# Kernel tuning notes

Measured on AMD Instinct MI355X. Metric: run time of the kernel, lower is better.

Reference implementation:

```python
import jax, jax.numpy as jnp
import numpy as np

N_NODES = 10000
AVG_DEG = 16
N_EDGES = N_NODES * AVG_DEG
NODE_DIM, EDGE_DIM, LIN_DIM, HID, OUT, LAYERS = 9, 3, 32, 300, 2, 5


def _init(key, shape, fan_in):
    return jax.random.normal(key, shape, jnp.float32) * (1.0 / np.sqrt(fan_in))


def setup_inputs() -> dict:
    key = jax.random.key(0)
    ks = jax.random.split(key, 18)
    inp = {
        "x": jax.random.normal(ks[0], (N_NODES, NODE_DIM), jnp.float32),
        "edge_index": jax.random.randint(ks[1], (2, N_EDGES), 0, N_NODES, jnp.int32),
        "edge_attr": jax.random.normal(ks[2], (N_EDGES, EDGE_DIM), jnp.float32),
        "batch": jnp.zeros((N_NODES,), jnp.int32),
        # nn.Linear params (stored as [in, out] so fwd is x @ W + b)
        "node_w": _init(ks[3], (NODE_DIM, LIN_DIM), NODE_DIM),
        "node_b": jnp.zeros((LIN_DIM,), jnp.float32),
        "edge_w": _init(ks[4], (EDGE_DIM, LIN_DIM), EDGE_DIM),
        "edge_b": jnp.zeros((LIN_DIM,), jnp.float32),
        # GCNConv: lin (no bias) + separate additive bias (PyG convention)
        "gcn0_w": _init(ks[5], (LIN_DIM, HID), LIN_DIM),
        "gcn0_b": jnp.zeros((HID,), jnp.float32),
        "gcn_w": _init(ks[6], (LAYERS - 1, HID, HID), HID),
        "gcn_b": jnp.zeros((LAYERS - 1, HID), jnp.float32),
        "lin1_w": _init(ks[7], (HID, LIN_DIM), HID),
        "lin1_b": jnp.zeros((LIN_DIM,), jnp.float32),
        "lin2_w": _init(ks[8], (LIN_DIM, OUT), LIN_DIM),
        "lin2_b": jnp.zeros((OUT,), jnp.float32),
    }
    return inp


def reference(x, edge_index, edge_attr, batch,
              node_w, node_b, edge_w, edge_b,
              gcn0_w, gcn0_b, gcn_w, gcn_b,
              lin1_w, lin1_b, lin2_w, lin2_b):
    row, col = edge_index[0], edge_index[1]

    e = edge_attr @ edge_w + edge_b  # [E, LIN_DIM] edge embeddings

    # Faithful to the original bug: node embeddings get edge attrs scatter-added,
    # then the result is discarded by `attr = edge_attr`. Kept for fidelity (dead).
    node_h = x @ node_w + node_b
    node_h = node_h.at[row].add(e)  # unused downstream

    # GCN stack runs over the E-row edge-embedding matrix -> effective node count = E
    h = e
    n = h.shape[0]  # == N_EDGES

    # symmetric gcn_norm with self-loops (edge_weight = 1), computed once
    deg = jax.ops.segment_sum(jnp.ones((edge_index.shape[1],), h.dtype), col,
                              num_segments=n) + 1.0
    dinv = jax.lax.rsqrt(deg)
    norm = dinv[row] * dinv[col]  # per-edge normalization
    self_norm = (dinv * dinv)[:, None]  # self-loop term

    def gcn(h, w, b):
        hw = h @ w  # dense transform
        agg = jax.ops.segment_sum(hw[row] * norm[:, None], col, num_segments=n)
        return agg + self_norm * hw + b

    h = jax.nn.relu(gcn(h, gcn0_w, gcn0_b))

    def step(h, wb):
        w, b = wb
        return jax.nn.relu(gcn(h, w, b)), None

    h, _ = jax.lax.scan(step, h, (gcn_w, gcn_b))

    g = jnp.mean(h, axis=0, keepdims=True)  # [1, HID] graph readout
    g = jax.nn.relu(g @ lin1_w + lin1_b)
    pred = g @ lin2_w + lin2_b  # [1, OUT]; forward returns pre-softmax logits
    return pred
```

## Files before the change

kernel.cpp:

```cpp
#include <hip/hip_runtime.h>
#include <hip/hip_bf16.h>

#define N_NODES 10000
#define N_EDGES 160000
#define HID 300
#define HIDP 304
#define NPARTB (N_EDGES - N_NODES)
#define KS 328
#define RBM 80
#define RBF 16
#define PARTB_BLOCKS 1875
#define GEMMA_BLOCKS 125
#define FILL_BLOCKS 313
#define MEGA_BLOCKS (PARTB_BLOCKS + GEMMA_BLOCKS + FILL_BLOCKS)
#define FUSE_BLOCKS 625

typedef __attribute__((ext_vector_type(8))) short short8;
typedef __attribute__((ext_vector_type(4))) short s16x4;
typedef __attribute__((ext_vector_type(4))) float f32x4;

#define MFMA_B16(a, b, c) __builtin_amdgcn_mfma_f32_16x16x32_bf16(a, b, c, 0, 0, 0)

__device__ __forceinline__ short bf16r(float x) {
    unsigned u = __float_as_uint(x);
    return (short)((u + 0x7fffu + ((u >> 16) & 1u)) >> 16);
}
__device__ __forceinline__ float b2f(unsigned short u) {
    return __uint_as_float(((unsigned)u) << 16);
}
__device__ __forceinline__ void split1(float x, short& hi, short& lo) {
    short h = bf16r(x);
    float hf = __uint_as_float(((unsigned)(unsigned short)h) << 16);
    hi = h;
    lo = bf16r(x - hf);
}

__global__ void k_prep(const float* __restrict__ g0w, const float* __restrict__ gw,
                       short* __restrict__ wt0, short* __restrict__ wtl,
                       const int* __restrict__ col, int* __restrict__ cnt) {
    int idx = blockIdx.x * 256 + threadIdx.x;
    if (idx < N_EDGES) atomicAdd(&cnt[col[idx]], 1);
    if (idx < 1216) {
        int n16 = idx & 15, q = (idx >> 4) & 3, nt = idx >> 6;
        int n = nt * 16 + n16;
        short* hd = wt0 + (size_t)(nt * 8 + q) * 128 + n16 * 8;
        short* ld = wt0 + (size_t)(nt * 8 + 4 + q) * 128 + n16 * 8;
#pragma unroll
        for (int j = 0; j < 8; ++j) {
            int k = q * 8 + j;
            float f = (n < HID) ? g0w[k * HID + n] : 0.0f;
            short hi, lo;
            split1(f, hi, lo);
            hd[j] = hi;
            ld[j] = lo;
        }
    } else if (idx < 1216 + 48640) {
        int i = idx - 1216;
        int n16 = i & 15; i >>= 4;
        int q = i & 3; i >>= 2;
        int nt = i % 19; i /= 19;
        int chunk = i % 10;
        int l = i / 10;
        int n = nt * 16 + n16;
        int cnt_idx = chunk * 19 + nt;
        short* base = wtl + (size_t)l * 194560;
        short* hd = base + (size_t)(cnt_idx * 8 + q) * 128 + n16 * 8;
        short* ld = base + (size_t)(cnt_idx * 8 + 4 + q) * 128 + n16 * 8;
#pragma unroll
        for (int j = 0; j < 8; ++j) {
            int k = chunk * 32 + q * 8 + j;
            float f = (k < HID && n < HID) ? gw[((size_t)l * HID + k) * HID + n] : 0.0f;
            short hi, lo;
            split1(f, hi, lo);
            hd[j] = hi;
            ld[j] = lo;
        }
    }
}

__global__ __launch_bounds__(1024) void k_scan(
    const int* __restrict__ cnt, int* __restrict__ col_start,
    int* __restrict__ cursor, float* __restrict__ dinv,
    float* __restrict__ selfnorm) {
    __shared__ int wsum[16];
    int t = threadIdx.x;
    int lane = t & 63, w = t >> 6;
    int carry = 0;
    for (int base = 0; base < N_NODES; base += 1024) {
        int i = base + t;
        int v = (i < N_NODES) ? cnt[i] : 0;
        int s = v;
#pragma unroll
        for (int d = 1; d < 64; d <<= 1) {
            int n = __shfl_up(s, d, 64);
            if (lane >= d) s += n;
        }
        if (lane == 63) wsum[w] = s;
        __syncthreads();
        int woff = 0, total = 0;
#pragma unroll
        for (int k = 0; k < 16; ++k) {
            if (k < w) woff += wsum[k];
            total += wsum[k];
        }
        if (i < N_NODES) {
            int excl = carry + woff + s - v;
            col_start[i] = excl;
            cursor[i] = excl;
            float dd = (float)v + 1.0f;
            dinv[i] = rsqrtf(dd);
            selfnorm[i] = 1.0f / dd;
        }
        carry += total;
        __syncthreads();
    }
    if (t == 0) col_start[N_NODES] = carry;
}

template <int MT, int NTC>
__device__ __forceinline__ void kloop(const short* __restrict__ wp, int nch,
                                      const short* Hh, int nt0, int quad, int l16,
                                      f32x4 (&acc)[MT][NTC]) {
#pragma unroll
    for (int mt = 0; mt < MT; ++mt)
#pragma unroll
        for (int i = 0; i < NTC; ++i)
#pragma unroll
            for (int r = 0; r < 4; ++r) acc[mt][i][r] = 0.0f;
#pragma unroll 1
    for (int c = 0; c < nch; ++c) {
        const short* cb = wp + (size_t)(c * 19 + nt0) * 1024 + quad * 128 + l16 * 8;
        short8 ah[MT];
#pragma unroll
        for (int mt = 0; mt < MT; ++mt)
            ah[mt] = *(const short8*)&Hh[(mt * 16 + l16) * KS + c * 32 + quad * 8];
        short8 bb[NTC];
#pragma unroll
        for (int i = 0; i < NTC; ++i) bb[i] = *(const short8*)(cb + (size_t)i * 1024);
#pragma unroll
        for (int mt = 0; mt < MT; ++mt)
#pragma unroll
            for (int i = 0; i < NTC; ++i)
                acc[mt][i] = MFMA_B16(ah[mt], bb[i], acc[mt][i]);
#pragma unroll
        for (int i = 0; i < NTC; ++i) bb[i] = *(const short8*)(cb + (size_t)i * 1024 + 512);
#pragma unroll
        for (int mt = 0; mt < MT; ++mt)
#pragma unroll
            for (int i = 0; i < NTC; ++i)
                acc[mt][i] = MFMA_B16(ah[mt], bb[i], acc[mt][i]);
    }
}

template <int MT, int NTC>
__device__ __forceinline__ void kloop_p(const short* __restrict__ wp, int nch,
                                        const short* Hh, int nt0, int quad, int l16,
                                        f32x4 (&acc)[MT][NTC]) {
#pragma unroll
    for (int mt = 0; mt < MT; ++mt)
#pragma unroll
        for (int i = 0; i < NTC; ++i)
#pragma unroll
            for (int r = 0; r < 4; ++r) acc[mt][i][r] = 0.0f;

    const short* a0 = Hh + l16 * KS + quad * 8;
    const short* w0 = wp + (size_t)nt0 * 1024 + (size_t)(quad * 128 + l16 * 8);

    short8 ah[MT], an[MT], b1[NTC], b1n[NTC], b2[NTC];
#pragma unroll
    for (int mt = 0; mt < MT; ++mt) ah[mt] = *(const short8*)(a0 + mt * 16 * KS);
#pragma unroll
    for (int i = 0; i < NTC; ++i) b1[i] = *(const short8*)(w0 + (size_t)i * 1024);

#pragma unroll 1
    for (int c = 0; c < nch - 1; ++c) {
        const short* wc = w0 + (size_t)c * 19456;
        const short* wn = wc + 19456;
        const short* apn = a0 + (c + 1) * 32;
#pragma unroll
        for (int i = 0; i < NTC; ++i) b2[i] = *(const short8*)(wc + (size_t)i * 1024 + 512);
#pragma unroll
        for (int mt = 0; mt < MT; ++mt) an[mt] = *(const short8*)(apn + mt * 16 * KS);
#pragma unroll
        for (int i = 0; i < NTC; ++i) b1n[i] = *(const short8*)(wn + (size_t)i * 1024);
#pragma unroll
        for (int mt = 0; mt < MT; ++mt)
#pragma unroll
            for (int i = 0; i < NTC; ++i) acc[mt][i] = MFMA_B16(ah[mt], b1[i], acc[mt][i]);
#pragma unroll
        for (int mt = 0; mt < MT; ++mt)
#pragma unroll
            for (int i = 0; i < NTC; ++i) acc[mt][i] = MFMA_B16(ah[mt], b2[i], acc[mt][i]);
#pragma unroll
        for (int mt = 0; mt < MT; ++mt) ah[mt] = an[mt];
#pragma unroll
        for (int i = 0; i < NTC; ++i) b1[i] = b1n[i];
    }
    {
        const short* wc = w0 + (size_t)(nch - 1) * 19456;
#pragma unroll
        for (int i = 0; i < NTC; ++i) b2[i] = *(const short8*)(wc + (size_t)i * 1024 + 512);
#pragma unroll
        for (int mt = 0; mt < MT; ++mt)
#pragma unroll
            for (int i = 0; i < NTC; ++i) acc[mt][i] = MFMA_B16(ah[mt], b1[i], acc[mt][i]);
#pragma unroll
        for (int mt = 0; mt < MT; ++mt)
#pragma unroll
            for (int i = 0; i < NTC; ++i) acc[mt][i] = MFMA_B16(ah[mt], b2[i], acc[mt][i]);
    }
}

template <int MT, int NTC>
__device__ __forceinline__ void gcn_epilogue(const float* __restrict__ bias,
                                             int nt0, int quad, int l16,
                                             f32x4 (&acc)[MT][NTC], short* Hh) {
#pragma unroll
    for (int i = 0; i < NTC; ++i) {
        int c = (nt0 + i) * 16 + l16;
        float b = (c < HID) ? bias[c] : 0.0f;
#pragma unroll
        for (int mt = 0; mt < MT; ++mt)
#pragma unroll
            for (int r = 0; r < 4; ++r) {
                float v = fmaxf(acc[mt][i][r] + b, 0.0f);
                Hh[(mt * 16 + quad * 4 + r) * KS + c] = bf16r(v);
            }
    }
}

template <int MT, int NTC>
__device__ __forceinline__ void gcn_final(const float* __restrict__ bias,
                                          int nt0, int quad, int l16,
                                          f32x4 (&acc)[MT][NTC],
                                          float* __restrict__ gout) {
#pragma unroll
    for (int i = 0; i < NTC; ++i) {
        int c = (nt0 + i) * 16 + l16;
        float b = (c < HID) ? bias[c] : 0.0f;
        float s = 0.0f;
#pragma unroll
        for (int mt = 0; mt < MT; ++mt)
#pragma unroll
            for (int r = 0; r < 4; ++r) s += fmaxf(acc[mt][i][r] + b, 0.0f);
        s += __shfl_xor(s, 16, 64);
        s += __shfl_xor(s, 32, 64);
        if (quad == 0) gout[c] = (c < HID) ? s : 0.0f;
    }
}

template <int MT, int NTC>
__device__ __forceinline__ void gemm_out(int base, int nt0, int quad, int l16,
                                         f32x4 (&acc)[MT][NTC],
                                         unsigned short* __restrict__ HW) {
#pragma unroll
    for (int i = 0; i < NTC; ++i) {
        int c = (nt0 + i) * 16 + l16;
#pragma unroll
        for (int mt = 0; mt < MT; ++mt)
#pragma unroll
            for (int r = 0; r < 4; ++r) {
                int gm = base + mt * 16 + quad * 4 + r;
                if (gm < N_NODES)
                    HW[(size_t)gm * HIDP + c] = (unsigned short)bf16r(acc[mt][i][r]);
            }
    }
}

__global__ __launch_bounds__(512, 4) void k_mega(
    const float* __restrict__ edge_attr,
    const float* __restrict__ edge_w,
    const float* __restrict__ edge_b,
    const short* __restrict__ wt0,
    const short* __restrict__ wtl,
    const float* __restrict__ gcn0_b,
    const float* __restrict__ gcn_b,
    float* __restrict__ gpartB,
    unsigned short* __restrict__ hw0,
    const int* __restrict__ row,
    const int* __restrict__ col,
    int* __restrict__ cursor,
    const float* __restrict__ dinv,
    int2* __restrict__ edge_pack) {
    __shared__ short Hh[RBM * KS];
    int bid = blockIdx.x, t = threadIdx.x;
    int lane = t & 63, w = t >> 6;
    int l16 = lane & 15, quad = lane >> 4;
    int nt0 = (w < 3) ? w * 3 : 9 + (w - 3) * 2;

    if (bid < PARTB_BLOCKS) {
        int base = N_NODES + bid * RBM;
        for (int i = t; i < RBM * 8; i += 512) {
            int r = i >> 3, c4 = (i & 7) * 4;
            const float* ar = edge_attr + (size_t)(base + r) * 3;
            float a0 = ar[0], a1 = ar[1], a2 = ar[2];
#pragma unroll
            for (int j = 0; j < 4; ++j) {
                int cc = c4 + j;
                float v = edge_b[cc];
                v = fmaf(a0, edge_w[cc], v);
                v = fmaf(a1, edge_w[32 + cc], v);
                v = fmaf(a2, edge_w[64 + cc], v);
                Hh[r * KS + cc] = bf16r(v);
            }
        }
        for (int i = t; i < RBM * 24; i += 512) {
            int r = i / 24, k = 304 + i % 24;
            Hh[r * KS + k] = 0;
        }
        __syncthreads();

        float* gout = gpartB + (size_t)bid * HIDP;
        if (w < 3) {
            f32x4 acc[5][3];
            kloop<5, 3>(wt0, 1, Hh, nt0, quad, l16, acc);
            __syncthreads();
            gcn_epilogue<5, 3>(gcn0_b, nt0, quad, l16, acc, Hh);
            __syncthreads();
            for (int l = 0; l < 4; ++l) {
                kloop<5, 3>(wtl + (size_t)l * 194560, 10, Hh, nt0, quad, l16, acc);
                __syncthreads();
                if (l < 3) {
                    gcn_epilogue<5, 3>(gcn_b + l * HID, nt0, quad, l16, acc, Hh);
                    __syncthreads();
                } else {
                    gcn_final<5, 3>(gcn_b + l * HID, nt0, quad, l16, acc, gout);
                }
            }
        } else {
            f32x4 acc[5][2];
            kloop<5, 2>(wt0, 1, Hh, nt0, quad, l16, acc);
            __syncthreads();
            gcn_epilogue<5, 2>(gcn0_b, nt0, quad, l16, acc, Hh);
            __syncthreads();
            for (int l = 0; l < 4; ++l) {
                kloop<5, 2>(wtl + (size_t)l * 194560, 10, Hh, nt0, quad, l16, acc);
                __syncthreads();
                if (l < 3) {
                    gcn_epilogue<5, 2>(gcn_b + l * HID, nt0, quad, l16, acc, Hh);
                    __syncthreads();
                } else {
                    gcn_final<5, 2>(gcn_b + l * HID, nt0, quad, l16, acc, gout);
                }
            }
        }
    } else if (bid < PARTB_BLOCKS + GEMMA_BLOCKS) {
        int base = (bid - PARTB_BLOCKS) * RBM;
        for (int i = t; i < RBM * 8; i += 512) {
            int r = i >> 3, c4 = (i & 7) * 4;
            const float* ar = edge_attr + (size_t)(base + r) * 3;
            float a0 = ar[0], a1 = ar[1], a2 = ar[2];
#pragma unroll
            for (int j = 0; j < 4; ++j) {
                int cc = c4 + j;
                float v = edge_b[cc];
                v = fmaf(a0, edge_w[cc], v);
                v = fmaf(a1, edge_w[32 + cc], v);
                v = fmaf(a2, edge_w[64 + cc], v);
                Hh[r * KS + cc] = bf16r(v);
            }
        }
        for (int i = t; i < RBM * 24; i += 512) {
            int r = i / 24, k = 304 + i % 24;
            Hh[r * KS + k] = 0;
        }
        __syncthreads();
        if (w < 3) {
            f32x4 acc[5][3];
            kloop<5, 3>(wt0, 1, Hh, nt0, quad, l16, acc);
            gemm_out<5, 3>(base, nt0, quad, l16, acc, hw0);
        } else {
            f32x4 acc[5][2];
            kloop<5, 2>(wt0, 1, Hh, nt0, quad, l16, acc);
            gemm_out<5, 2>(base, nt0, quad, l16, acc, hw0);
        }
    } else {
        int e = (bid - PARTB_BLOCKS - GEMMA_BLOCKS) * 512 + t;
        if (e < N_EDGES) {
            int c = col[e], r = row[e];
            int p = atomicAdd(&cursor[c], 1);
            edge_pack[p] = make_int2(r, __float_as_int(dinv[r] * dinv[c]));
        }
    }
}

__device__ __forceinline__ void agg_edge4(int i, int lane, int cap,
                                          const unsigned short* __restrict__ hw_in,
                                          const int2* __restrict__ ep,
                                          float (&v)[5]) {
    int2 e0 = ep[i], e1 = ep[i + 1], e2 = ep[i + 2], e3 = ep[i + 3];
    const unsigned short* h0 = hw_in + (size_t)e0.x * HIDP;
    const unsigned short* h1 = hw_in + (size_t)e1.x * HIDP;
    const unsigned short* h2 = hw_in + (size_t)e2.x * HIDP;
    const unsigned short* h3 = hw_in + (size_t)e3.x * HIDP;
    float n0 = __int_as_float(e0.y), n1 = __int_as_float(e1.y);
    float n2 = __int_as_float(e2.y), n3 = __int_as_float(e3.y);
#pragma unroll
    for (int jj = 0; jj < 5; ++jj) {
        int cc = lane + 64 * jj;
        if (cc < cap) {
            float s = v[jj];
            s = fmaf(n0, b2f(h0[cc]), s);
            s = fmaf(n1, b2f(h1[cc]), s);
            s = fmaf(n2, b2f(h2[cc]), s);
            s = fmaf(n3, b2f(h3[cc]), s);
            v[jj] = s;
        }
    }
}

__device__ __forceinline__ void agg_pair(int c0, int c1, int lane,
                                         const unsigned short* __restrict__ hw_in,
                                         const int* __restrict__ col_start,
                                         const int2* __restrict__ ep,
                                         float (&v0)[5], float (&v1)[5]) {
#pragma unroll
    for (int jj = 0; jj < 5; ++jj) { v0[jj] = 0.0f; v1[jj] = 0.0f; }
    int i0 = col_start[c0], e0 = col_start[c0 + 1];
    int i1 = col_start[c1], e1 = col_start[c1 + 1];
#pragma unroll 1
    while (i0 + 4 <= e0 && i1 + 4 <= e1) {
        int2 a0 = ep[i0], a1 = ep[i0 + 1], a2 = ep[i0 + 2], a3 = ep[i0 + 3];
        int2 b0 = ep[i1], b1 = ep[i1 + 1], b2 = ep[i1 + 2], b3 = ep[i1 + 3];
        const unsigned short* pa0 = hw_in + (size_t)a0.x * HIDP;
        const unsigned short* pa1 = hw_in + (size_t)a1.x * HIDP;
        const unsigned short* pa2 = hw_in + (size_t)a2.x * HIDP;
        const unsigned short* pa3 = hw_in + (size_t)a3.x * HIDP;
        const unsigned short* pb0 = hw_in + (size_t)b0.x * HIDP;
        const unsigned short* pb1 = hw_in + (size_t)b1.x * HIDP;
        const unsigned short* pb2 = hw_in + (size_t)b2.x * HIDP;
        const unsigned short* pb3 = hw_in + (size_t)b3.x * HIDP;
        float na0 = __int_as_float(a0.y), na1 = __int_as_float(a1.y);
        float na2 = __int_as_float(a2.y), na3 = __int_as_float(a3.y);
        float nb0 = __int_as_float(b0.y), nb1 = __int_as_float(b1.y);
        float nb2 = __int_as_float(b2.y), nb3 = __int_as_float(b3.y);
#pragma unroll
        for (int jj = 0; jj < 5; ++jj) {
            int cc = lane + 64 * jj;
            if (cc < HIDP) {
                float s = v0[jj];
                s = fmaf(na0, b2f(pa0[cc]), s);
                s = fmaf(na1, b2f(pa1[cc]), s);
                s = fmaf(na2, b2f(pa2[cc]), s);
                s = fmaf(na3, b2f(pa3[cc]), s);
                v0[jj] = s;
                float u = v1[jj];
                u = fmaf(nb0, b2f(pb0[cc]), u);
                u = fmaf(nb1, b2f(pb1[cc]), u);
                u = fmaf(nb2, b2f(pb2[cc]), u);
                u = fmaf(nb3, b2f(pb3[cc]), u);
                v1[jj] = u;
            }
        }
        i0 += 4; i1 += 4;
    }
#pragma unroll 1
    for (; i0 + 4 <= e0; i0 += 4) agg_edge4(i0, lane, HIDP, hw_in, ep, v0);
#pragma unroll 1
    for (; i0 < e0; ++i0) {
        int2 q = ep[i0];
        const unsigned short* h = hw_in + (size_t)q.x * HIDP;
        float n = __int_as_float(q.y);
#pragma unroll
        for (int jj = 0; jj < 5; ++jj) {
            int cc = lane + 64 * jj;
            if (cc < HIDP) v0[jj] = fmaf(n, b2f(h[cc]), v0[jj]);
        }
    }
#pragma unroll 1
    for (; i1 + 4 <= e1; i1 += 4) agg_edge4(i1, lane, HIDP, hw_in, ep, v1);
#pragma unroll 1
    for (; i1 < e1; ++i1) {
        int2 q = ep[i1];
        const unsigned short* h = hw_in + (size_t)q.x * HIDP;
        float n = __int_as_float(q.y);
#pragma unroll
        for (int jj = 0; jj < 5; ++jj) {
            int cc = lane + 64 * jj;
            if (cc < HIDP) v1[jj] = fmaf(n, b2f(h[cc]), v1[jj]);
        }
    }
}

__global__ __launch_bounds__(512, 4) void k_fuse(
    const unsigned short* __restrict__ hw_in,
    const int* __restrict__ col_start,
    const int2* __restrict__ edge_pack,
    const float* __restrict__ selfnorm,
    const float* __restrict__ bias,
    const short* __restrict__ wt,
    unsigned short* __restrict__ hw_out) {
    __shared__ short Hh[RBF * KS];
    int t = threadIdx.x;
    int lane = t & 63, w = t >> 6;
    int l16 = lane & 15, quad = lane >> 4;
    int base = blockIdx.x * RBF;
    int nt0 = (w < 3) ? w * 3 : 9 + (w - 3) * 2;

    {
        int c0 = base + w * 2, c1 = c0 + 1;
        float v0[5], v1[5];
        agg_pair(c0, c1, lane, hw_in, col_start, edge_pack, v0, v1);
        float sn0 = selfnorm[c0], sn1 = selfnorm[c1];
        const unsigned short* sp0 = hw_in + (size_t)c0 * HIDP;
        const unsigned short* sp1 = hw_in + (size_t)c1 * HIDP;
        int r0 = w * 2;
#pragma unroll
        for (int jj = 0; jj < 5; ++jj) {
            int cc = lane + 64 * jj;
            if (cc < HIDP) {
                float b = (cc < HID) ? bias[cc] : 0.0f;
                float h0 = v0[jj] + sn0 * b2f(sp0[cc]) + b;
                float h1 = v1[jj] + sn1 * b2f(sp1[cc]) + b;
                Hh[r0 * KS + cc] = bf16r(fmaxf(h0, 0.0f));
                Hh[(r0 + 1) * KS + cc] = bf16r(fmaxf(h1, 0.0f));
            }
        }
    }
    for (int i = t; i < RBF * 6; i += 512) {
        int r = i / 6, k = 304 + (i % 6) * 4;
        *(s16x4*)&Hh[r * KS + k] = (s16x4)0;
    }
    __syncthreads();

    if (w < 3) {
        f32x4 acc[1][3];
        kloop_p<1, 3>(wt, 10, Hh, nt0, quad, l16, acc);
        gemm_out<1, 3>(base, nt0, quad, l16, acc, hw_out);
    } else {
        f32x4 acc[1][2];
        kloop_p<1, 2>(wt, 10, Hh, nt0, quad, l16, acc);
        gemm_out<1, 2>(base, nt0, quad, l16, acc, hw_out);
    }
}

__global__ __launch_bounds__(512) void k_last(
    const unsigned short* __restrict__ hw_in,
    const int* __restrict__ col_start,
    const int2* __restrict__ edge_pack,
    const float* __restrict__ selfnorm,
    const float* __restrict__ bias,
    const float* __restrict__ gpartB,
    float* __restrict__ g_sum) {
    __shared__ float red[8 * 320];
    int t = threadIdx.x;
    int lane = t & 63, w = t >> 6;
    int base = blockIdx.x * RBF;

    float s[5] = {0.0f, 0.0f, 0.0f, 0.0f, 0.0f};
    {
        int c0 = base + w * 2, c1 = c0 + 1;
        float v0[5], v1[5];
        agg_pair(c0, c1, lane, hw_in, col_start, edge_pack, v0, v1);
        float sn0 = selfnorm[c0], sn1 = selfnorm[c1];
        const unsigned short* sp0 = hw_in + (size_t)c0 * HIDP;
        const unsigned short* sp1 = hw_in + (size_t)c1 * HIDP;
#pragma unroll
        for (int jj = 0; jj < 5; ++jj) {
            int cc = lane + 64 * jj;
            if (cc < HID) {
                float b = bias[cc];
                s[jj] += fmaxf(v0[jj] + sn0 * b2f(sp0[cc]) + b, 0.0f);
                s[jj] += fmaxf(v1[jj] + sn1 * b2f(sp1[cc]) + b, 0.0f);
            }
        }
    }
    if (w < 3) {
        int rr = blockIdx.x * 3 + w;
        if (rr < PARTB_BLOCKS) {
#pragma unroll
            for (int jj = 0; jj < 5; ++jj) {
                int cc = lane + 64 * jj;
                if (cc < HID) s[jj] += gpartB[(size_t)rr * HIDP + cc];
            }
        }
    }
#pragma unroll
    for (int jj = 0; jj < 5; ++jj) red[w * 320 + lane + 64 * jj] = s[jj];
    __syncthreads();
    if (w == 0) {
#pragma unroll
        for (int jj = 0; jj < 5; ++jj) {
            int cc = lane + 64 * jj;
            if (cc < HID) {
                float tot = 0.0f;
#pragma unroll
                for (int g = 0; g < 8; ++g) tot += red[g * 320 + cc];
                atomicAdd(&g_sum[cc], tot);
            }
        }
    }
}

__global__ void k_head(const float* __restrict__ g_sum,
                       const float* __restrict__ lin1_w, const float* __restrict__ lin1_b,
                       const float* __restrict__ lin2_w, const float* __restrict__ lin2_b,
                       float* __restrict__ out) {
    __shared__ float g2[32];
    int t = threadIdx.x;
    const float inv = 1.0f / (float)N_EDGES;
    if (t < 32) {
        float a = lin1_b[t];
        for (int d = 0; d < HID; ++d) a = fmaf(g_sum[d] * inv, lin1_w[d * 32 + t], a);
        g2[t] = fmaxf(a, 0.0f);
    }
    __syncthreads();
    if (t < 2) {
        float p = lin2_b[t];
        for (int j = 0; j < 32; ++j) p = fmaf(g2[j], lin2_w[j * 2 + t], p);
        out[t] = p;
    }
}


extern "C" void kernel_launch(void* const* d_in, const int* in_sizes, int n_in,
                              void* d_out, int out_size, void* d_ws, size_t ws_size,
                              hipStream_t stream) {
    (void)in_sizes; (void)n_in; (void)out_size; (void)ws_size;
    const int* edge_index = (const int*)d_in[1];
    const float* edge_attr = (const float*)d_in[2];
    const float* edge_w = (const float*)d_in[6];
    const float* edge_b = (const float*)d_in[7];
    const float* gcn0_w = (const float*)d_in[8];
    const float* gcn0_b = (const float*)d_in[9];
    const float* gcn_w = (const float*)d_in[10];
    const float* gcn_b = (const float*)d_in[11];
    const float* lin1_w = (const float*)d_in[12];
    const float* lin1_b = (const float*)d_in[13];
    const float* lin2_w = (const float*)d_in[14];
    const float* lin2_b = (const float*)d_in[15];

    char* ws = (char*)d_ws;
    size_t off = 0;
    auto alloc = [&](size_t bytes) {
        void* p = ws + off;
        off = (off + bytes + 255) & ~(size_t)255;
        return p;
    };
    unsigned short* hwA = (unsigned short*)alloc((size_t)N_NODES * HIDP * 2);
    unsigned short* hwB = (unsigned short*)alloc((size_t)N_NODES * HIDP * 2);
    int2* edge_pack = (int2*)alloc((size_t)N_EDGES * 8);
    int* cnt = (int*)alloc((size_t)N_NODES * 4);
    int* col_start = (int*)alloc((size_t)(N_NODES + 1) * 4);
    int* cursor = (int*)alloc((size_t)N_NODES * 4);
    float* dinv = (float*)alloc((size_t)N_NODES * 4);
    float* selfnorm = (float*)alloc((size_t)N_NODES * 4);
    float* g_sum = (float*)alloc((size_t)HIDP * 4);
    short* wt0 = (short*)alloc((size_t)38912);
    short* wtl = (short*)alloc((size_t)4 * 389120);
    float* gpartB = (float*)alloc((size_t)PARTB_BLOCKS * HIDP * 4);

    const int* row = edge_index;
    const int* col = edge_index + N_EDGES;

    hipMemsetAsync(cnt, 0, N_NODES * 4, stream);
    hipMemsetAsync(g_sum, 0, HIDP * 4, stream);

    k_prep<<<(N_EDGES + 255) / 256, 256, 0, stream>>>(gcn0_w, gcn_w, wt0, wtl, col, cnt);
    k_scan<<<1, 1024, 0, stream>>>(cnt, col_start, cursor, dinv, selfnorm);

    k_mega<<<MEGA_BLOCKS, 512, 0, stream>>>(edge_attr, edge_w, edge_b, wt0, wtl,
                                            gcn0_b, gcn_b, gpartB, hwA,
                                            row, col, cursor, dinv, edge_pack);

    k_fuse<<<FUSE_BLOCKS, 512, 0, stream>>>(hwA, col_start, edge_pack, selfnorm,
                                            gcn0_b, wtl + (size_t)0 * 194560, hwB);
    k_fuse<<<FUSE_BLOCKS, 512, 0, stream>>>(hwB, col_start, edge_pack, selfnorm,
                                            gcn_b + 0 * HID, wtl + (size_t)1 * 194560, hwA);
    k_fuse<<<FUSE_BLOCKS, 512, 0, stream>>>(hwA, col_start, edge_pack, selfnorm,
                                            gcn_b + 1 * HID, wtl + (size_t)2 * 194560, hwB);
    k_fuse<<<FUSE_BLOCKS, 512, 0, stream>>>(hwB, col_start, edge_pack, selfnorm,
                                            gcn_b + 2 * HID, wtl + (size_t)3 * 194560, hwA);
    k_last<<<FUSE_BLOCKS, 512, 0, stream>>>(hwA, col_start, edge_pack, selfnorm,
                                            gcn_b + 3 * HID, gpartB, g_sum);
    k_head<<<1, 64, 0, stream>>>(g_sum, lin1_w, lin1_b, lin2_w, lin2_b, (float*)d_out);
}
```

Baseline: 460.1 us.

## Interleave independent partB dense-GCN blocks with the four aggregation layer kernels

```diff
diff --git a/kernel.cpp b/kernel.cpp
--- a/kernel.cpp
+++ b/kernel.cpp
@@ -5,15 +5,15 @@
 #define N_EDGES 160000
 #define HID 300
 #define HIDP 304
-#define NPARTB (N_EDGES - N_NODES)
 #define KS 328
 #define RBM 80
 #define RBF 16
 #define PARTB_BLOCKS 1875
 #define GEMMA_BLOCKS 125
 #define FILL_BLOCKS 313
-#define MEGA_BLOCKS (PARTB_BLOCKS + GEMMA_BLOCKS + FILL_BLOCKS)
+#define PRE_BLOCKS (GEMMA_BLOCKS + FILL_BLOCKS)
 #define FUSE_BLOCKS 625
+#define MIX_BLOCKS 1099
 
 typedef __attribute__((ext_vector_type(8))) short short8;
 typedef __attribute__((ext_vector_type(4))) short s16x4;
@@ -267,15 +267,74 @@
     }
 }
 
-__global__ __launch_bounds__(512, 4) void k_mega(
+__device__ __forceinline__ void partB_unit(
+    int pb, int t, int w, int lane, int l16, int quad, int nt0,
+    const float* __restrict__ edge_attr, const float* __restrict__ edge_w,
+    const float* __restrict__ edge_b, const short* __restrict__ wt0,
+    const short* __restrict__ wtl, const float* __restrict__ gcn0_b,
+    const float* __restrict__ gcn_b, float* __restrict__ gpartB, short* Hh) {
+    int base = N_NODES + pb * RBM;
+    for (int i = t; i < RBM * 8; i += 512) {
+        int r = i >> 3, c4 = (i & 7) * 4;
+        const float* ar = edge_attr + (size_t)(base + r) * 3;
+        float a0 = ar[0], a1 = ar[1], a2 = ar[2];
+#pragma unroll
+        for (int j = 0; j < 4; ++j) {
+            int cc = c4 + j;
+            float v = edge_b[cc];
+            v = fmaf(a0, edge_w[cc], v);
+            v = fmaf(a1, edge_w[32 + cc], v);
+            v = fmaf(a2, edge_w[64 + cc], v);
+            Hh[r * KS + cc] = bf16r(v);
+        }
+    }
+    for (int i = t; i < RBM * 24; i += 512) {
+        int r = i / 24, k = 304 + i % 24;
+        Hh[r * KS + k] = 0;
+    }
+    __syncthreads();
+
+    float* gout = gpartB + (size_t)pb * HIDP;
+    if (w < 3) {
+        f32x4 acc[5][3];
+        kloop<5, 3>(wt0, 1, Hh, nt0, quad, l16, acc);
+        __syncthreads();
+        gcn_epilogue<5, 3>(gcn0_b, nt0, quad, l16, acc, Hh);
+        __syncthreads();
+        for (int l = 0; l < 4; ++l) {
+            kloop<5, 3>(wtl + (size_t)l * 194560, 10, Hh, nt0, quad, l16, acc);
+            __syncthreads();
+            if (l < 3) {
+                gcn_epilogue<5, 3>(gcn_b + l * HID, nt0, quad, l16, acc, Hh);
+                __syncthreads();
+            } else {
+                gcn_final<5, 3>(gcn_b + l * HID, nt0, quad, l16, acc, gout);
+            }
+        }
+    } else {
+        f32x4 acc[5][2];
+        kloop<5, 2>(wt0, 1, Hh, nt0, quad, l16, acc);
+        __syncthreads();
+        gcn_epilogue<5, 2>(gcn0_b, nt0, quad, l16, acc, Hh);
+        __syncthreads();
+        for (int l = 0; l < 4; ++l) {
+            kloop<5, 2>(wtl + (size_t)l * 194560, 10, Hh, nt0, quad, l16, acc);
+            __syncthreads();
+            if (l < 3) {
+                gcn_epilogue<5, 2>(gcn_b + l * HID, nt0, quad, l16, acc, Hh);
+                __syncthreads();
+            } else {
+                gcn_final<5, 2>(gcn_b + l * HID, nt0, quad, l16, acc, gout);
+            }
+        }
+    }
+}
+
+__global__ __launch_bounds__(512, 4) void k_pre(
     const float* __restrict__ edge_attr,
     const float* __restrict__ edge_w,
     const float* __restrict__ edge_b,
     const short* __restrict__ wt0,
-    const short* __restrict__ wtl,
-    const float* __restrict__ gcn0_b,
-    const float* __restrict__ gcn_b,
-    float* __restrict__ gpartB,
     unsigned short* __restrict__ hw0,
     const int* __restrict__ row,
     const int* __restrict__ col,
@@ -288,64 +347,8 @@
     int l16 = lane & 15, quad = lane >> 4;
     int nt0 = (w < 3) ? w * 3 : 9 + (w - 3) * 2;
 
-    if (bid < PARTB_BLOCKS) {
-        int base = N_NODES + bid * RBM;
-        for (int i = t; i < RBM * 8; i += 512) {
-            int r = i >> 3, c4 = (i & 7) * 4;
-            const float* ar = edge_attr + (size_t)(base + r) * 3;
-            float a0 = ar[0], a1 = ar[1], a2 = ar[2];
-#pragma unroll
-            for (int j = 0; j < 4; ++j) {
-                int cc = c4 + j;
-                float v = edge_b[cc];
-                v = fmaf(a0, edge_w[cc], v);
-                v = fmaf(a1, edge_w[32 + cc], v);
-                v = fmaf(a2, edge_w[64 + cc], v);
-                Hh[r * KS + cc] = bf16r(v);
-            }
-        }
-        for (int i = t; i < RBM * 24; i += 512) {
-            int r = i / 24, k = 304 + i % 24;
-            Hh[r * KS + k] = 0;
-        }
-        __syncthreads();
-
-        float* gout = gpartB + (size_t)bid * HIDP;
-        if (w < 3) {
-            f32x4 acc[5][3];
-            kloop<5, 3>(wt0, 1, Hh, nt0, quad, l16, acc);
-            __syncthreads();
-            gcn_epilogue<5, 3>(gcn0_b, nt0, quad, l16, acc, Hh);
-            __syncthreads();
-            for (int l = 0; l < 4; ++l) {
-                kloop<5, 3>(wtl + (size_t)l * 194560, 10, Hh, nt0, quad, l16, acc);
-                __syncthreads();
-                if (l < 3) {
-                    gcn_epilogue<5, 3>(gcn_b + l * HID, nt0, quad, l16, acc, Hh);
-                    __syncthreads();
-                } else {
-                    gcn_final<5, 3>(gcn_b + l * HID, nt0, quad, l16, acc, gout);
-                }
-            }
-        } else {
-            f32x4 acc[5][2];
-            kloop<5, 2>(wt0, 1, Hh, nt0, quad, l16, acc);
-            __syncthreads();
-            gcn_epilogue<5, 2>(gcn0_b, nt0, quad, l16, acc, Hh);
-            __syncthreads();
-            for (int l = 0; l < 4; ++l) {
-                kloop<5, 2>(wtl + (size_t)l * 194560, 10, Hh, nt0, quad, l16, acc);
-                __syncthreads();
-                if (l < 3) {
-                    gcn_epilogue<5, 2>(gcn_b + l * HID, nt0, quad, l16, acc, Hh);
-                    __syncthreads();
-                } else {
-                    gcn_final<5, 2>(gcn_b + l * HID, nt0, quad, l16, acc, gout);
-                }
-            }
-        }
-    } else if (bid < PARTB_BLOCKS + GEMMA_BLOCKS) {
-        int base = (bid - PARTB_BLOCKS) * RBM;
+    if (bid < GEMMA_BLOCKS) {
+        int base = bid * RBM;
         for (int i = t; i < RBM * 8; i += 512) {
             int r = i >> 3, c4 = (i & 7) * 4;
             const float* ar = edge_attr + (size_t)(base + r) * 3;
@@ -375,7 +378,7 @@
             gemm_out<5, 2>(base, nt0, quad, l16, acc, hw0);
         }
     } else {
-        int e = (bid - PARTB_BLOCKS - GEMMA_BLOCKS) * 512 + t;
+        int e = (bid - GEMMA_BLOCKS) * 512 + t;
         if (e < N_EDGES) {
             int c = col[e], r = row[e];
             int p = atomicAdd(&cursor[c], 1);
@@ -384,7 +387,7 @@
     }
 }
 
-__device__ __forceinline__ void agg_edge4(int i, int lane, int cap,
+__device__ __forceinline__ void agg_edge4(int i, int lane,
                                           const unsigned short* __restrict__ hw_in,
                                           const int2* __restrict__ ep,
                                           float (&v)[5]) {
@@ -398,7 +401,7 @@
 #pragma unroll
     for (int jj = 0; jj < 5; ++jj) {
         int cc = lane + 64 * jj;
-        if (cc < cap) {
+        if (cc < HIDP) {
             float s = v[jj];
             s = fmaf(n0, b2f(h0[cc]), s);
             s = fmaf(n1, b2f(h1[cc]), s);
@@ -455,7 +458,7 @@
         i0 += 4; i1 += 4;
     }
 #pragma unroll 1
-    for (; i0 + 4 <= e0; i0 += 4) agg_edge4(i0, lane, HIDP, hw_in, ep, v0);
+    for (; i0 + 4 <= e0; i0 += 4) agg_edge4(i0, lane, hw_in, ep, v0);
 #pragma unroll 1
     for (; i0 < e0; ++i0) {
         int2 q = ep[i0];
@@ -468,7 +471,7 @@
         }
     }
 #pragma unroll 1
-    for (; i1 + 4 <= e1; i1 += 4) agg_edge4(i1, lane, HIDP, hw_in, ep, v1);
+    for (; i1 + 4 <= e1; i1 += 4) agg_edge4(i1, lane, hw_in, ep, v1);
 #pragma unroll 1
     for (; i1 < e1; ++i1) {
         int2 q = ep[i1];
@@ -482,55 +485,74 @@
     }
 }
 
-__global__ __launch_bounds__(512, 4) void k_fuse(
+__global__ __launch_bounds__(512, 4) void k_mix(
     const unsigned short* __restrict__ hw_in,
     const int* __restrict__ col_start,
     const int2* __restrict__ edge_pack,
     const float* __restrict__ selfnorm,
     const float* __restrict__ bias,
     const short* __restrict__ wt,
-    unsigned short* __restrict__ hw_out) {
-    __shared__ short Hh[RBF * KS];
-    int t = threadIdx.x;
+    unsigned short* __restrict__ hw_out,
+    const float* __restrict__ edge_attr,
+    const float* __restrict__ edge_w,
+    const float* __restrict__ edge_b,
+    const short* __restrict__ wt0,
+    const short* __restrict__ wtl,
+    const float* __restrict__ gcn0_b,
+    const float* __restrict__ gcn_b,
+    float* __restrict__ gpartB,
+    int pbase, int pcount) {
+    __shared__ short Hh[RBM * KS];
+    int bid = blockIdx.x, t = threadIdx.x;
     int lane = t & 63, w = t >> 6;
     int l16 = lane & 15, quad = lane >> 4;
-    int base = blockIdx.x * RBF;
     int nt0 = (w < 3) ? w * 3 : 9 + (w - 3) * 2;
 
-    {
-        int c0 = base + w * 2, c1 = c0 + 1;
-        float v0[5], v1[5];
-        agg_pair(c0, c1, lane, hw_in, col_start, edge_pack, v0, v1);
-        float sn0 = selfnorm[c0], sn1 = selfnorm[c1];
-        const unsigned short* sp0 = hw_in + (size_t)c0 * HIDP;
-        const unsigned short* sp1 = hw_in + (size_t)c1 * HIDP;
-        int r0 = w * 2;
-#pragma unroll
-        for (int jj = 0; jj < 5; ++jj) {
-            int cc = lane + 64 * jj;
-            if (cc < HIDP) {
-                float b = (cc < HID) ? bias[cc] : 0.0f;
-                float h0 = v0[jj] + sn0 * b2f(sp0[cc]) + b;
-                float h1 = v1[jj] + sn1 * b2f(sp1[cc]) + b;
-                Hh[r0 * KS + cc] = bf16r(fmaxf(h0, 0.0f));
-                Hh[(r0 + 1) * KS + cc] = bf16r(fmaxf(h1, 0.0f));
-            }
-        }
-    }
-    for (int i = t; i < RBF * 6; i += 512) {
-        int r = i / 6, k = 304 + (i % 6) * 4;
-        *(s16x4*)&Hh[r * KS + k] = (s16x4)0;
-    }
-    __syncthreads();
-
-    if (w < 3) {
-        f32x4 acc[1][3];
-        kloop_p<1, 3>(wt, 10, Hh, nt0, quad, l16, acc);
-        gemm_out<1, 3>(base, nt0, quad, l16, acc, hw_out);
+    int kk = bid / 7, r7 = bid % 7;
+    if (r7 < 3) {
+        int pidx = kk * 3 + r7;
+        if (pidx >= pcount) return;
+        partB_unit(pbase + pidx, t, w, lane, l16, quad, nt0,
+                   edge_attr, edge_w, edge_b, wt0, wtl, gcn0_b, gcn_b, gpartB, Hh);
     } else {
-        f32x4 acc[1][2];
-        kloop_p<1, 2>(wt, 10, Hh, nt0, quad, l16, acc);
-        gemm_out<1, 2>(base, nt0, quad, l16, acc, hw_out);
+        int gidx = kk * 4 + (r7 - 3);
+        if (gidx >= FUSE_BLOCKS) return;
+        int base = gidx * RBF;
+        {
+            int c0 = base + w * 2, c1 = c0 + 1;
+            float v0[5], v1[5];
+            agg_pair(c0, c1, lane, hw_in, col_start, edge_pack, v0, v1);
+            float sn0 = selfnorm[c0], sn1 = selfnorm[c1];
+            const unsigned short* sp0 = hw_in + (size_t)c0 * HIDP;
+            const unsigned short* sp1 = hw_in + (size_t)c1 * HIDP;
+            int r0 = w * 2;
+#pragma unroll
+            for (int jj = 0; jj < 5; ++jj) {
+                int cc = lane + 64 * jj;
+                if (cc < HIDP) {
+                    float b = (cc < HID) ? bias[cc] : 0.0f;
+                    float h0 = v0[jj] + sn0 * b2f(sp0[cc]) + b;
+                    float h1 = v1[jj] + sn1 * b2f(sp1[cc]) + b;
+                    Hh[r0 * KS + cc] = bf16r(fmaxf(h0, 0.0f));
+                    Hh[(r0 + 1) * KS + cc] = bf16r(fmaxf(h1, 0.0f));
+                }
+            }
+        }
+        for (int i = t; i < RBF * 6; i += 512) {
+            int r = i / 6, k = 304 + (i % 6) * 4;
+            *(s16x4*)&Hh[r * KS + k] = (s16x4)0;
+        }
+        __syncthreads();
+
+        if (w < 3) {
+            f32x4 acc[1][3];
+            kloop_p<1, 3>(wt, 10, Hh, nt0, quad, l16, acc);
+            gemm_out<1, 3>(base, nt0, quad, l16, acc, hw_out);
+        } else {
+            f32x4 acc[1][2];
+            kloop_p<1, 2>(wt, 10, Hh, nt0, quad, l16, acc);
+            gemm_out<1, 2>(base, nt0, quad, l16, acc, hw_out);
+        }
     }
 }
 
@@ -659,18 +681,25 @@
     k_prep<<<(N_EDGES + 255) / 256, 256, 0, stream>>>(gcn0_w, gcn_w, wt0, wtl, col, cnt);
     k_scan<<<1, 1024, 0, stream>>>(cnt, col_start, cursor, dinv, selfnorm);
 
-    k_mega<<<MEGA_BLOCKS, 512, 0, stream>>>(edge_attr, edge_w, edge_b, wt0, wtl,
-                                            gcn0_b, gcn_b, gpartB, hwA,
-                                            row, col, cursor, dinv, edge_pack);
-
-    k_fuse<<<FUSE_BLOCKS, 512, 0, stream>>>(hwA, col_start, edge_pack, selfnorm,
-                                            gcn0_b, wtl + (size_t)0 * 194560, hwB);
-    k_fuse<<<FUSE_BLOCKS, 512, 0, stream>>>(hwB, col_start, edge_pack, selfnorm,
-                                            gcn_b + 0 * HID, wtl + (size_t)1 * 194560, hwA);
-    k_fuse<<<FUSE_BLOCKS, 512, 0, stream>>>(hwA, col_start, edge_pack, selfnorm,
-                                            gcn_b + 1 * HID, wtl + (size_t)2 * 194560, hwB);
-    k_fuse<<<FUSE_BLOCKS, 512, 0, stream>>>(hwB, col_start, edge_pack, selfnorm,
-                                            gcn_b + 2 * HID, wtl + (size_t)3 * 194560, hwA);
+    k_pre<<<PRE_BLOCKS, 512, 0, stream>>>(edge_attr, edge_w, edge_b, wt0, hwA,
+                                          row, col, cursor, dinv, edge_pack);
+
+    k_mix<<<MIX_BLOCKS, 512, 0, stream>>>(hwA, col_start, edge_pack, selfnorm,
+                                          gcn0_b, wtl + (size_t)0 * 194560, hwB,
+                                          edge_attr, edge_w, edge_b, wt0, wtl,
+                                          gcn0_b, gcn_b, gpartB, 0, 469);
+    k_mix<<<MIX_BLOCKS, 512, 0, stream>>>(hwB, col_start, edge_pack, selfnorm,
+                                          gcn_b + 0 * HID, wtl + (size_t)1 * 194560, hwA,
+                                          edge_attr, edge_w, edge_b, wt0, wtl,
+                                          gcn0_b, gcn_b, gpartB, 469, 469);
+    k_mix<<<MIX_BLOCKS, 512, 0, stream>>>(hwA, col_start, edge_pack, selfnorm,
+                                          gcn_b + 1 * HID, wtl + (size_t)2 * 194560, hwB,
+                                          edge_attr, edge_w, edge_b, wt0, wtl,
+                                          gcn0_b, gcn_b, gpartB, 938, 469);
+    k_mix<<<MIX_BLOCKS, 512, 0, stream>>>(hwB, col_start, edge_pack, selfnorm,
+                                          gcn_b + 2 * HID, wtl + (size_t)3 * 194560, hwA,
+                                          edge_attr, edge_w, edge_b, wt0, wtl,
+                                          gcn0_b, gcn_b, gpartB, 1407, 468);
     k_last<<<FUSE_BLOCKS, 512, 0, stream>>>(hwA, col_start, edge_pack, selfnorm,
                                             gcn_b + 3 * HID, gpartB, g_sum);
     k_head<<<1, 64, 0, stream>>>(g_sum, lin1_w, lin1_b, lin2_w, lin2_b, (float*)d_out);
```

New measurement: 498.5 us. 1.08x slower.
